# Kernel optimization log

Hardware: AMD Instinct MI355X
Metric: run time of the kernel (lower is better)

The kernel has to match this reference:

```python
import jax, jax.numpy as jnp
import numpy as np

EPS = 1e-5  # torch LayerNorm default

def layernorm(x, g, b):
    mu = jnp.mean(x, axis=-1, keepdims=True)
    var = jnp.mean(jnp.square(x - mu), axis=-1, keepdims=True)
    return (x - mu) * jax.lax.rsqrt(var + EPS) * g + b

def setup_inputs() -> dict:
    key = jax.random.key(0)
    ks = jax.random.split(key, 12)
    B, L1, L2 = 8, 2048, 2048
    D1, D2, E = 1024, 768, 1024
    s1, s2, se = D1 ** -0.5, D2 ** -0.5, E ** -0.5
    return {
        "modality1": jax.random.normal(ks[0], (B, L1, D1), jnp.float32),
        "modality2": jax.random.normal(ks[1], (B, L2, D2), jnp.float32),
        "ln1_g": jnp.ones((D1,), jnp.float32),
        "ln1_b": jnp.zeros((D1,), jnp.float32),
        "ln2_g": jnp.ones((D2,), jnp.float32),
        "ln2_b": jnp.zeros((D2,), jnp.float32),
        "Wq": jax.random.normal(ks[2], (D1, E), jnp.float32) * s1,
        "bq": jax.random.normal(ks[3], (E,), jnp.float32) * 0.01,
        "Wk": jax.random.normal(ks[4], (D2, E), jnp.float32) * s2,
        "bk": jax.random.normal(ks[5], (E,), jnp.float32) * 0.01,
        "Wv": jax.random.normal(ks[6], (D2, E), jnp.float32) * s2,
        "bv": jax.random.normal(ks[7], (E,), jnp.float32) * 0.01,
        "Wo": jax.random.normal(ks[8], (E, D1), jnp.float32) * se,
        "bo": jax.random.normal(ks[9], (D1,), jnp.float32) * 0.01,
    }

def reference(modality1, modality2, ln1_g, ln1_b, ln2_g, ln2_b,
              Wq, bq, Wk, bk, Wv, bv, Wo, bo):
    E = Wq.shape[1]
    scaling = E ** -0.5
    x1 = layernorm(modality1, ln1_g, ln1_b)   # [B, L1, D1]
    x2 = layernorm(modality2, ln2_g, ln2_b)   # [B, L2, D2]
    q = x1 @ Wq + bq                           # [B, L1, E]
    k = x2 @ Wk + bk                           # [B, L2, E]
    v = x2 @ Wv + bv                           # [B, L2, E]
    scores = jnp.einsum('bqe,bke->bqk', q, k) * scaling
    attn = jax.nn.softmax(scores, axis=-1)     # [B, L1, L2]
    ctx = jnp.einsum('bqk,bke->bqe', attn, v)  # [B, L1, E]
    return ctx @ Wo + bo                        # [B, L1, D1]
```

## Files before the change

kernel.cpp:

```cpp
#include <hip/hip_runtime.h>
#include <hip/hip_bf16.h>

typedef __bf16 bf16_t;
typedef __bf16 bf16x4_t __attribute__((ext_vector_type(4)));
typedef __bf16 bf16x8_t __attribute__((ext_vector_type(8)));
typedef float f32x4_t __attribute__((ext_vector_type(4)));
typedef float f32x16_t __attribute__((ext_vector_type(16)));

typedef __attribute__((address_space(1))) void gvoid_t;
typedef __attribute__((address_space(3))) void svoid_t;

__device__ __forceinline__ void gload_lds16(const void* g, void* s) {
    __builtin_amdgcn_global_load_lds((gvoid_t*)g, (svoid_t*)s, 16, 0, 0);
}

__device__ __forceinline__ void wg_barrier() {
    asm volatile("" ::: "memory");
    __builtin_amdgcn_s_barrier();
    asm volatile("" ::: "memory");
}

template <typename CT, bool BIAS, bool STORE_T = false>
__global__ __launch_bounds__(512, 2)
void gemm_bt(const bf16_t* __restrict__ A, const bf16_t* __restrict__ Bt,
             CT* __restrict__ C, const float* __restrict__ bias,
             int M, int N, int K, float scale,
             size_t sA, size_t sB, size_t sC, int tshift)
{
    __shared__ bf16_t As[2 * 256 * 64];
    __shared__ bf16_t Bs[2 * 256 * 64];

    const int nx = gridDim.x, ny = gridDim.y;
    const int nblk = nx * ny * (int)gridDim.z;
    int lin = blockIdx.x + nx * (blockIdx.y + ny * blockIdx.z);
    int tile = lin;
    if ((nblk & 7) == 0)
        tile = (lin & 7) * (nblk >> 3) + (lin >> 3);
    const int per_z = nx * ny;
    const int bz = tile / per_z;
    int t = tile - bz * per_z;
    const int SB = 8;
    const int band = t / (nx * SB);
    const int r = t - band * (nx * SB);
    const int h = min(SB, ny - band * SB);
    const int bx = r / h;
    const int by = band * SB + (r - bx * h);

    A  += (size_t)bz * sA;
    Bt += (size_t)bz * sB;
    C  += (size_t)bz * sC;

    const int tid  = threadIdx.x;
    const int wave = tid >> 6;
    const int lane = tid & 63;
    const int m0 = by * 256;
    const int n0 = bx * 256;

    const int srow = tid >> 3;
    const int lc8  = ((tid & 7) ^ (srow & 7)) * 8;
    const bf16_t* Ag = A  + (size_t)(m0 + srow) * K + lc8;
    const bf16_t* Bg = Bt + (size_t)(n0 + srow) * K + lc8;
    const size_t rs = (size_t)64 * K;
    const int sbase = wave * 512;

    const int wm = wave >> 2;
    const int wn = wave & 3;
    const int lr = lane & 31;
    const int kh = lane >> 5;
    const int rsw = lr & 7;

    f32x16_t acc[4][2];
#pragma unroll
    for (int i = 0; i < 4; ++i)
#pragma unroll
        for (int j = 0; j < 2; ++j)
            acc[i][j] = (f32x16_t)(0.f);

    const int NT = K >> 6;

    auto stage = [&](int buf) {
        bf16_t* a = As + buf * 16384;
        bf16_t* b = Bs + buf * 16384;
        const bf16_t* ap = Ag;
        const bf16_t* bp = Bg;
#pragma unroll
        for (int j = 0; j < 4; ++j) {
            gload_lds16(ap, a + j * 4096 + sbase);
            gload_lds16(bp, b + j * 4096 + sbase);
            ap += rs; bp += rs;
        }
        Ag += 64; Bg += 64;
    };

    stage(0);
    asm volatile("s_waitcnt vmcnt(0)" ::: "memory");
    wg_barrier();

    for (int kt = 0; kt < NT; ++kt) {
        const int buf = kt & 1;
        if (kt + 1 < NT) stage(buf ^ 1);

        const bf16_t* ab = As + buf * 16384;
        const bf16_t* bb = Bs + buf * 16384;

#pragma unroll
        for (int kp = 0; kp < 2; ++kp) {
            bf16x8_t bfr[2][2];
#pragma unroll
            for (int nj = 0; nj < 2; ++nj)
#pragma unroll
                for (int kq = 0; kq < 2; ++kq)
                    bfr[nj][kq] = *(const bf16x8_t*)
                        &bb[(wn * 64 + nj * 32 + lr) * 64 +
                            (((kp * 2 + kq) * 2 + kh) ^ rsw) * 8];
#pragma unroll
            for (int mp = 0; mp < 2; ++mp) {
                bf16x8_t af[2][2];
#pragma unroll
                for (int mq = 0; mq < 2; ++mq)
#pragma unroll
                    for (int kq = 0; kq < 2; ++kq)
                        af[mq][kq] = *(const bf16x8_t*)
                            &ab[(wm * 128 + (mp * 2 + mq) * 32 + lr) * 64 +
                                (((kp * 2 + kq) * 2 + kh) ^ rsw) * 8];
                __builtin_amdgcn_s_setprio(1);
#pragma unroll
                for (int mq = 0; mq < 2; ++mq)
#pragma unroll
                    for (int nj = 0; nj < 2; ++nj)
#pragma unroll
                        for (int kq = 0; kq < 2; ++kq)
                            acc[mp * 2 + mq][nj] =
                                __builtin_amdgcn_mfma_f32_32x32x16_bf16(
                                    af[mq][kq], bfr[nj][kq],
                                    acc[mp * 2 + mq][nj], 0, 0, 0);
                __builtin_amdgcn_s_setprio(0);
            }
        }

        asm volatile("s_waitcnt vmcnt(0) lgkmcnt(0)" ::: "memory");
        wg_barrier();
    }

#pragma unroll
    for (int nj = 0; nj < 2; ++nj) {
        const int col = n0 + wn * 64 + nj * 32 + lr;
        const float bv = BIAS ? bias[col] : 0.0f;
#pragma unroll
        for (int mi = 0; mi < 4; ++mi) {
            f32x16_t v = acc[mi][nj];
#pragma unroll
            for (int g = 0; g < 4; ++g) {
                const int row = m0 + wm * 128 + mi * 32 + 8 * g + 4 * kh;
                if constexpr (STORE_T) {
                    const int b = row >> tshift;
                    const int l = row & ((1 << tshift) - 1);
                    bf16x4_t o;
#pragma unroll
                    for (int rr2 = 0; rr2 < 4; ++rr2)
                        o[rr2] = (bf16_t)(v[g * 4 + rr2] * scale + bv);
                    *(bf16x4_t*)((bf16_t*)C + ((size_t)b * N << tshift) +
                                 ((size_t)col << tshift) + l) = o;
                } else {
#pragma unroll
                    for (int rr2 = 0; rr2 < 4; ++rr2) {
                        float val = v[g * 4 + rr2] * scale + bv;
                        C[(size_t)(row + rr2) * N + col] = (CT)val;
                    }
                }
            }
        }
    }
}

template <int NV>
__global__ __launch_bounds__(256, 4)
void layernorm_k(const float* __restrict__ x, const float* __restrict__ g,
                 const float* __restrict__ b, bf16_t* __restrict__ y)
{
    const int D = NV * 256;
    const int wave = threadIdx.x >> 6, lane = threadIdx.x & 63;
    const size_t row = (size_t)blockIdx.x * 4 + wave;
    const float4* xr = (const float4*)(x + row * D);

    float4 v[NV];
    float s = 0.f, sq = 0.f;
#pragma unroll
    for (int i = 0; i < NV; ++i) {
        v[i] = xr[lane + 64 * i];
        s  += v[i].x + v[i].y + v[i].z + v[i].w;
        sq += v[i].x * v[i].x + v[i].y * v[i].y + v[i].z * v[i].z + v[i].w * v[i].w;
    }
#pragma unroll
    for (int m = 32; m; m >>= 1) {
        s  += __shfl_xor(s, m, 64);
        sq += __shfl_xor(sq, m, 64);
    }
    const float mean = s / D;
    const float rstd = rsqrtf(fmaxf(sq / D - mean * mean, 0.f) + 1e-5f);

#pragma unroll
    for (int i = 0; i < NV; ++i) {
        const int c4 = lane + 64 * i;
        float4 gg = ((const float4*)g)[c4];
        float4 bb = ((const float4*)b)[c4];
        bf16x4_t o;
        o[0] = (bf16_t)((v[i].x - mean) * rstd * gg.x + bb.x);
        o[1] = (bf16_t)((v[i].y - mean) * rstd * gg.y + bb.y);
        o[2] = (bf16_t)((v[i].z - mean) * rstd * gg.z + bb.z);
        o[3] = (bf16_t)((v[i].w - mean) * rstd * gg.w + bb.w);
        *(bf16x4_t*)(y + row * D + (size_t)c4 * 4) = o;
    }
}

__global__ __launch_bounds__(256, 4)
void softmax_rows(bf16_t* __restrict__ a)
{
    const int wave = threadIdx.x >> 6, lane = threadIdx.x & 63;
    const size_t row = (size_t)blockIdx.x * 4 + wave;
    bf16_t* r = a + row * 2048;

    float v[32];
    float mx = -3.0e38f;
#pragma unroll
    for (int i = 0; i < 4; ++i) {
        bf16x8_t t = *(const bf16x8_t*)(r + (size_t)(lane + 64 * i) * 8);
#pragma unroll
        for (int j = 0; j < 8; ++j) {
            v[i * 8 + j] = (float)t[j];
            mx = fmaxf(mx, v[i * 8 + j]);
        }
    }
#pragma unroll
    for (int m = 32; m; m >>= 1) mx = fmaxf(mx, __shfl_xor(mx, m, 64));
    float s = 0.f;
#pragma unroll
    for (int i = 0; i < 32; ++i) { v[i] = __expf(v[i] - mx); s += v[i]; }
#pragma unroll
    for (int m = 32; m; m >>= 1) s += __shfl_xor(s, m, 64);
    const float rs = 1.0f / s;
#pragma unroll
    for (int i = 0; i < 4; ++i) {
        bf16x8_t t;
#pragma unroll
        for (int j = 0; j < 8; ++j) t[j] = (bf16_t)(v[i * 8 + j] * rs);
        *(bf16x8_t*)(r + (size_t)(lane + 64 * i) * 8) = t;
    }
}

__global__ __launch_bounds__(256, 4)
void wconvT(const float* __restrict__ w, bf16_t* __restrict__ wt, int K, int N)
{
    __shared__ float s[32][33];
    const int tx = threadIdx.x, ty = threadIdx.y;
    const int n0 = blockIdx.x * 32, k0 = blockIdx.y * 32;
#pragma unroll
    for (int r = 0; r < 4; ++r)
        s[ty + r * 8][tx] = w[(size_t)(k0 + ty + r * 8) * N + n0 + tx];
    __syncthreads();
#pragma unroll
    for (int r = 0; r < 4; ++r)
        wt[(size_t)(n0 + ty + r * 8) * K + k0 + tx] = (bf16_t)s[tx][ty + r * 8];
}


extern "C" void kernel_launch(void* const* d_in, const int* in_sizes, int n_in,
                              void* d_out, int out_size, void* d_ws, size_t ws_size,
                              hipStream_t stream)
{
    const int B = 8, L1 = 2048, L2 = 2048, D1 = 1024, D2 = 768, E = 1024;
    const float scale = 0.03125f;
    const int tsh = 11;

    const float* m1   = (const float*)d_in[0];
    const float* m2   = (const float*)d_in[1];
    const float* ln1g = (const float*)d_in[2];
    const float* ln1b = (const float*)d_in[3];
    const float* ln2g = (const float*)d_in[4];
    const float* ln2b = (const float*)d_in[5];
    const float* Wq   = (const float*)d_in[6];
    const float* bq   = (const float*)d_in[7];
    const float* Wk   = (const float*)d_in[8];
    const float* bk   = (const float*)d_in[9];
    const float* Wv   = (const float*)d_in[10];
    const float* bv   = (const float*)d_in[11];
    const float* Wo   = (const float*)d_in[12];
    const float* bo   = (const float*)d_in[13];
    float* out = (float*)d_out;

    bf16_t* ws = (bf16_t*)d_ws;
    size_t off = 0;
    auto alloc = [&](size_t n) { bf16_t* p = ws + off; off += n; return p; };
    bf16_t* WqT = alloc((size_t)E * D1);
    bf16_t* WkT = alloc((size_t)E * D2);
    bf16_t* WvT = alloc((size_t)E * D2);
    bf16_t* WoT = alloc((size_t)D1 * E);
    bf16_t* x1  = alloc((size_t)B * L1 * D1);
    bf16_t* x2  = alloc((size_t)B * L2 * D2);
    bf16_t* Qb  = alloc((size_t)B * L1 * E);
    bf16_t* Kb  = alloc((size_t)B * L2 * E);
    bf16_t* VTb = alloc((size_t)B * E * L2);
    bf16_t* ctx = alloc((size_t)B * L1 * E);
    bf16_t* attn = ws + off;
    const bool batched = (off + (size_t)B * L1 * L2) * sizeof(bf16_t) <= ws_size;

    dim3 blk256(256);
    dim3 blk512(512);

    wconvT<<<dim3(E / 32, D1 / 32), dim3(32, 8), 0, stream>>>(Wq, WqT, D1, E);
    wconvT<<<dim3(E / 32, D2 / 32), dim3(32, 8), 0, stream>>>(Wk, WkT, D2, E);
    wconvT<<<dim3(E / 32, D2 / 32), dim3(32, 8), 0, stream>>>(Wv, WvT, D2, E);
    wconvT<<<dim3(D1 / 32, E / 32), dim3(32, 8), 0, stream>>>(Wo, WoT, E, D1);

    layernorm_k<4><<<dim3(B * L1 / 4), blk256, 0, stream>>>(m1, ln1g, ln1b, x1);
    layernorm_k<3><<<dim3(B * L2 / 4), blk256, 0, stream>>>(m2, ln2g, ln2b, x2);

    gemm_bt<bf16_t, true><<<dim3(E / 256, B * L1 / 256, 1), blk512, 0, stream>>>(
        x1, WqT, Qb, bq, B * L1, E, D1, 1.0f, 0, 0, 0, 0);
    gemm_bt<bf16_t, true><<<dim3(E / 256, B * L2 / 256, 1), blk512, 0, stream>>>(
        x2, WkT, Kb, bk, B * L2, E, D2, 1.0f, 0, 0, 0, 0);
    gemm_bt<bf16_t, true, true><<<dim3(E / 256, B * L2 / 256, 1), blk512, 0, stream>>>(
        x2, WvT, VTb, bv, B * L2, E, D2, 1.0f, 0, 0, 0, tsh);

    if (batched) {
        gemm_bt<bf16_t, false><<<dim3(L2 / 256, L1 / 256, B), blk512, 0, stream>>>(
            Qb, Kb, attn, nullptr, L1, L2, E, scale,
            (size_t)L1 * E, (size_t)L2 * E, (size_t)L1 * L2, 0);
        softmax_rows<<<dim3(B * L1 / 4), blk256, 0, stream>>>(attn);
        gemm_bt<bf16_t, false><<<dim3(E / 256, L1 / 256, B), blk512, 0, stream>>>(
            attn, VTb, ctx, nullptr, L1, E, L2, 1.0f,
            (size_t)L1 * L2, (size_t)E * L2, (size_t)L1 * E, 0);
    } else {
        for (int b = 0; b < B; ++b) {
            gemm_bt<bf16_t, false><<<dim3(L2 / 256, L1 / 256, 1), blk512, 0, stream>>>(
                Qb + (size_t)b * L1 * E, Kb + (size_t)b * L2 * E, attn, nullptr,
                L1, L2, E, scale, 0, 0, 0, 0);
            softmax_rows<<<dim3(L1 / 4), blk256, 0, stream>>>(attn);
            gemm_bt<bf16_t, false><<<dim3(E / 256, L1 / 256, 1), blk512, 0, stream>>>(
                attn, VTb + (size_t)b * E * L2, ctx + (size_t)b * L1 * E, nullptr,
                L1, E, L2, 1.0f, 0, 0, 0, 0);
        }
    }

    gemm_bt<float, true><<<dim3(D1 / 256, B * L1 / 256, 1), blk512, 0, stream>>>(
        ctx, WoT, out, bo, B * L1, D1, E, 1.0f, 0, 0, 0, 0);
}
```

Measured before the change: 514.5 us.

## Switch GEMM to 16x16x32 MFMA with quadrant-interleaved staged pipeline

Rewrites the bf16 GEMM main loop to use 16x16x32 MFMA fragments instead of 32x32x16. It splits each K-tile into four quadrant sub-steps, and each sub-step issues half-tile global-to-LDS loads for tiles up to two iterations ahead, with finer vmcnt/lgkmcnt waits and sched barriers. The aim is to overlap global loads and LDS reads with MFMA work and to avoid the full drain barrier of the old loop. In exchange it adds more barriers per tile and changes the accumulator layout and epilogue, which risks extra synchronisation overhead and higher register pressure.

```diff
diff --git a/kernel.cpp b/kernel.cpp
--- a/kernel.cpp
+++ b/kernel.cpp
@@ -5,7 +5,6 @@
 typedef __bf16 bf16x4_t __attribute__((ext_vector_type(4)));
 typedef __bf16 bf16x8_t __attribute__((ext_vector_type(8)));
 typedef float f32x4_t __attribute__((ext_vector_type(4)));
-typedef float f32x16_t __attribute__((ext_vector_type(16)));
 
 typedef __attribute__((address_space(1))) void gvoid_t;
 typedef __attribute__((address_space(3))) void svoid_t;
@@ -27,8 +26,8 @@
              int M, int N, int K, float scale,
              size_t sA, size_t sB, size_t sC, int tshift)
 {
-    __shared__ bf16_t As[2 * 256 * 64];
-    __shared__ bf16_t Bs[2 * 256 * 64];
+    __shared__ __align__(16) bf16_t As[2 * 256 * 64];
+    __shared__ __align__(16) bf16_t Bs[2 * 256 * 64];
 
     const int nx = gridDim.x, ny = gridDim.y;
     const int nblk = nx * ny * (int)gridDim.z;
@@ -38,10 +37,10 @@
         tile = (lin & 7) * (nblk >> 3) + (lin >> 3);
     const int per_z = nx * ny;
     const int bz = tile / per_z;
-    int t = tile - bz * per_z;
+    int t0 = tile - bz * per_z;
     const int SB = 8;
-    const int band = t / (nx * SB);
-    const int r = t - band * (nx * SB);
+    const int band = t0 / (nx * SB);
+    const int r = t0 - band * (nx * SB);
     const int h = min(SB, ny - band * SB);
     const int bx = r / h;
     const int by = band * SB + (r - bx * h);
@@ -60,113 +59,136 @@
     const int lc8  = ((tid & 7) ^ (srow & 7)) * 8;
     const bf16_t* Ag = A  + (size_t)(m0 + srow) * K + lc8;
     const bf16_t* Bg = Bt + (size_t)(n0 + srow) * K + lc8;
-    const size_t rs = (size_t)64 * K;
+    const size_t h64 = (size_t)64 * K;
     const int sbase = wave * 512;
 
     const int wm = wave >> 2;
     const int wn = wave & 3;
-    const int lr = lane & 31;
-    const int kh = lane >> 5;
-    const int rsw = lr & 7;
-
-    f32x16_t acc[4][2];
-#pragma unroll
-    for (int i = 0; i < 4; ++i)
-#pragma unroll
-        for (int j = 0; j < 2; ++j)
-            acc[i][j] = (f32x16_t)(0.f);
+    const int fl = lane & 15;
+    const int fh = lane >> 4;
+    const int rsw = lane & 7;
+
+    f32x4_t acc[8][4];
+#pragma unroll
+    for (int i = 0; i < 8; ++i)
+#pragma unroll
+        for (int j = 0; j < 4; ++j)
+            acc[i][j] = (f32x4_t)(0.f);
 
     const int NT = K >> 6;
 
-    auto stage = [&](int buf) {
-        bf16_t* a = As + buf * 16384;
-        bf16_t* b = Bs + buf * 16384;
-        const bf16_t* ap = Ag;
-        const bf16_t* bp = Bg;
-#pragma unroll
-        for (int j = 0; j < 4; ++j) {
-            gload_lds16(ap, a + j * 4096 + sbase);
-            gload_lds16(bp, b + j * 4096 + sbase);
-            ap += rs; bp += rs;
+    auto stage_half = [&](int op, int kt, int hh) {
+        if (kt >= NT) return;
+        const bf16_t* src = (op ? Bg : Ag) + (size_t)kt * 64 + (size_t)(hh * 2) * h64;
+        bf16_t* dst = (op ? Bs : As) + ((kt & 1) * 16384 + hh * 8192 + sbase);
+        gload_lds16(src, dst);
+        gload_lds16(src + h64, dst + 4096);
+    };
+
+    bf16x8_t af[2][4][2];
+    bf16x8_t bf[2][2];
+
+#define RD_A(QM, BO)                                                           \
+    _Pragma("unroll") for (int mi = 0; mi < 4; ++mi)                           \
+    _Pragma("unroll") for (int kk = 0; kk < 2; ++kk)                           \
+        af[QM][mi][kk] = *(const bf16x8_t*)&As[(BO) +                          \
+            (wm * 128 + (QM) * 64 + mi * 16 + fl) * 64 +                       \
+            ((kk * 4 + fh) ^ rsw) * 8];
+
+#define RD_B(QN, BO)                                                           \
+    _Pragma("unroll") for (int nj = 0; nj < 2; ++nj)                           \
+    _Pragma("unroll") for (int kk = 0; kk < 2; ++kk)                           \
+        bf[nj][kk] = *(const bf16x8_t*)&Bs[(BO) +                              \
+            (wn * 64 + (QN) * 32 + nj * 16 + fl) * 64 +                        \
+            ((kk * 4 + fh) ^ rsw) * 8];
+
+#define MM(QM, QN)                                                             \
+    __builtin_amdgcn_s_setprio(1);                                             \
+    _Pragma("unroll") for (int mi = 0; mi < 4; ++mi)                           \
+    _Pragma("unroll") for (int nj = 0; nj < 2; ++nj)                           \
+    _Pragma("unroll") for (int kk = 0; kk < 2; ++kk)                           \
+        acc[(QM) * 4 + mi][(QN) * 2 + nj] =                                    \
+            __builtin_amdgcn_mfma_f32_16x16x32_bf16(                           \
+                af[QM][mi][kk], bf[nj][kk],                                    \
+                acc[(QM) * 4 + mi][(QN) * 2 + nj], 0, 0, 0);                   \
+    __builtin_amdgcn_s_setprio(0);
+
+#define LGKM0_PIN()                                                            \
+    asm volatile("s_waitcnt lgkmcnt(0)" ::: "memory");                         \
+    __builtin_amdgcn_sched_barrier(0);
+
+    stage_half(0, 0, 0); stage_half(0, 0, 1);
+    stage_half(1, 0, 0); stage_half(1, 0, 1);
+    stage_half(0, 1, 0); stage_half(0, 1, 1);
+    asm volatile("s_waitcnt vmcnt(4)" ::: "memory");
+    __builtin_amdgcn_sched_barrier(0);
+    wg_barrier();
+
+    for (int u = 0; u < NT; ++u) {
+        const int bo = (u & 1) * 16384;
+
+        RD_A(0, bo)
+        RD_B(0, bo)
+        stage_half(1, u + 1, 0);
+        asm volatile("s_waitcnt lgkmcnt(8)" ::: "memory");
+        wg_barrier();
+        LGKM0_PIN()
+        MM(0, 0)
+        wg_barrier();
+
+        RD_A(1, bo)
+        stage_half(1, u + 1, 1);
+        wg_barrier();
+        LGKM0_PIN()
+        MM(1, 0)
+        wg_barrier();
+
+        RD_B(1, bo)
+        stage_half(0, u + 2, 0);
+        wg_barrier();
+        LGKM0_PIN()
+        MM(0, 1)
+        wg_barrier();
+
+        stage_half(0, u + 2, 1);
+        if (u + 2 < NT) {
+            asm volatile("s_waitcnt vmcnt(4)" ::: "memory");
+        } else {
+            asm volatile("s_waitcnt vmcnt(0)" ::: "memory");
         }
-        Ag += 64; Bg += 64;
-    };
-
-    stage(0);
-    asm volatile("s_waitcnt vmcnt(0)" ::: "memory");
-    wg_barrier();
-
-    for (int kt = 0; kt < NT; ++kt) {
-        const int buf = kt & 1;
-        if (kt + 1 < NT) stage(buf ^ 1);
-
-        const bf16_t* ab = As + buf * 16384;
-        const bf16_t* bb = Bs + buf * 16384;
-
-#pragma unroll
-        for (int kp = 0; kp < 2; ++kp) {
-            bf16x8_t bfr[2][2];
-#pragma unroll
-            for (int nj = 0; nj < 2; ++nj)
-#pragma unroll
-                for (int kq = 0; kq < 2; ++kq)
-                    bfr[nj][kq] = *(const bf16x8_t*)
-                        &bb[(wn * 64 + nj * 32 + lr) * 64 +
-                            (((kp * 2 + kq) * 2 + kh) ^ rsw) * 8];
-#pragma unroll
-            for (int mp = 0; mp < 2; ++mp) {
-                bf16x8_t af[2][2];
-#pragma unroll
-                for (int mq = 0; mq < 2; ++mq)
-#pragma unroll
-                    for (int kq = 0; kq < 2; ++kq)
-                        af[mq][kq] = *(const bf16x8_t*)
-                            &ab[(wm * 128 + (mp * 2 + mq) * 32 + lr) * 64 +
-                                (((kp * 2 + kq) * 2 + kh) ^ rsw) * 8];
-                __builtin_amdgcn_s_setprio(1);
-#pragma unroll
-                for (int mq = 0; mq < 2; ++mq)
-#pragma unroll
-                    for (int nj = 0; nj < 2; ++nj)
-#pragma unroll
-                        for (int kq = 0; kq < 2; ++kq)
-                            acc[mp * 2 + mq][nj] =
-                                __builtin_amdgcn_mfma_f32_32x32x16_bf16(
-                                    af[mq][kq], bfr[nj][kq],
-                                    acc[mp * 2 + mq][nj], 0, 0, 0);
-                __builtin_amdgcn_s_setprio(0);
-            }
-        }
-
-        asm volatile("s_waitcnt vmcnt(0) lgkmcnt(0)" ::: "memory");
-        wg_barrier();
-    }
-
-#pragma unroll
-    for (int nj = 0; nj < 2; ++nj) {
-        const int col = n0 + wn * 64 + nj * 32 + lr;
+        __builtin_amdgcn_sched_barrier(0);
+        wg_barrier();
+        MM(1, 1)
+        wg_barrier();
+    }
+
+#undef RD_A
+#undef RD_B
+#undef MM
+#undef LGKM0_PIN
+
+#pragma unroll
+    for (int nf = 0; nf < 4; ++nf) {
+        const int col = n0 + wn * 64 + nf * 16 + fl;
         const float bv = BIAS ? bias[col] : 0.0f;
 #pragma unroll
-        for (int mi = 0; mi < 4; ++mi) {
-            f32x16_t v = acc[mi][nj];
-#pragma unroll
-            for (int g = 0; g < 4; ++g) {
-                const int row = m0 + wm * 128 + mi * 32 + 8 * g + 4 * kh;
-                if constexpr (STORE_T) {
-                    const int b = row >> tshift;
-                    const int l = row & ((1 << tshift) - 1);
-                    bf16x4_t o;
-#pragma unroll
-                    for (int rr2 = 0; rr2 < 4; ++rr2)
-                        o[rr2] = (bf16_t)(v[g * 4 + rr2] * scale + bv);
-                    *(bf16x4_t*)((bf16_t*)C + ((size_t)b * N << tshift) +
-                                 ((size_t)col << tshift) + l) = o;
-                } else {
-#pragma unroll
-                    for (int rr2 = 0; rr2 < 4; ++rr2) {
-                        float val = v[g * 4 + rr2] * scale + bv;
-                        C[(size_t)(row + rr2) * N + col] = (CT)val;
-                    }
+        for (int mf = 0; mf < 8; ++mf) {
+            f32x4_t v = acc[mf][nf];
+            const int row0 = m0 + wm * 128 + mf * 16 + fh * 4;
+            if constexpr (STORE_T) {
+                const int b = row0 >> tshift;
+                const int l = row0 & ((1 << tshift) - 1);
+                bf16x4_t o;
+#pragma unroll
+                for (int rr2 = 0; rr2 < 4; ++rr2)
+                    o[rr2] = (bf16_t)(v[rr2] * scale + bv);
+                *(bf16x4_t*)((bf16_t*)C + ((size_t)b * N << tshift) +
+                             ((size_t)col << tshift) + l) = o;
+            } else {
+#pragma unroll
+                for (int rr2 = 0; rr2 < 4; ++rr2) {
+                    float val = v[rr2] * scale + bv;
+                    C[(size_t)(row0 + rr2) * N + col] = (CT)val;
                 }
             }
         }
```

Result: slower. 528.1 us (+2.6%).
